# Optimization experiments

Measured on AMD Instinct MI355X. Metric: run time of the kernel, lower is better.

The kernel has to match this reference:

```python
import jax, jax.numpy as jnp
import numpy as np

D_MODEL = 1024
NUM_HEADS = 16
DIM_KEY = D_MODEL // NUM_HEADS
B, S = 2, 2048


def setup_inputs() -> dict:
    key = jax.random.key(0)
    ks = jax.random.split(key, 11)
    s = 1.0 / np.sqrt(D_MODEL)
    inp = {
        "query": jax.random.normal(ks[0], (B, S, D_MODEL), jnp.float32),
        "key": jax.random.normal(ks[1], (B, S, D_MODEL), jnp.float32),
        "value": jax.random.normal(ks[2], (B, S, D_MODEL), jnp.float32),
        "W_q": jax.random.uniform(ks[3], (D_MODEL, D_MODEL), jnp.float32, -s, s),
        "b_q": jax.random.uniform(ks[4], (D_MODEL,), jnp.float32, -s, s),
        "W_k": jax.random.uniform(ks[5], (D_MODEL, D_MODEL), jnp.float32, -s, s),
        "b_k": jax.random.uniform(ks[6], (D_MODEL,), jnp.float32, -s, s),
        "W_v": jax.random.uniform(ks[7], (D_MODEL, D_MODEL), jnp.float32, -s, s),
        "b_v": jax.random.uniform(ks[8], (D_MODEL,), jnp.float32, -s, s),
        "W_o": jax.random.uniform(ks[9], (D_MODEL, D_MODEL), jnp.float32, -s, s),
        "b_o": jax.random.uniform(ks[10], (D_MODEL,), jnp.float32, -s, s),
    }
    return inp


def _split_heads(x):
    # [B, S, D] -> [B, H, S, dk]
    b, s, _ = x.shape
    return x.reshape(b, s, NUM_HEADS, DIM_KEY).transpose(0, 2, 1, 3)


def reference(query, key, value, W_q, b_q, W_k, b_k, W_v, b_v, W_o, b_o):
    # torch Linear: y = x @ W^T + b
    q = _split_heads(query @ W_q.T + b_q)   # [B,H,S,dk]
    k = _split_heads(key @ W_k.T + b_k)
    v = _split_heads(value @ W_v.T + b_v)
    scale = 1.0 / np.sqrt(DIM_KEY).astype(np.float32)
    scores = jnp.einsum("bhqd,bhkd->bhqk", q, k) * scale  # [B,H,S,S]
    probs = jax.nn.softmax(scores, axis=-1)
    attn = jnp.einsum("bhqk,bhkd->bhqd", probs, v)        # [B,H,S,dk]
    combined = attn.transpose(0, 2, 1, 3).reshape(query.shape[0], query.shape[1], D_MODEL)
    return combined @ W_o.T + b_o
```

## Files before the change

kernel.cpp:

```cpp
#include <hip/hip_runtime.h>
#include <stdint.h>


typedef float f32x4 __attribute__((ext_vector_type(4)));
typedef __bf16 bf16x8 __attribute__((ext_vector_type(8)));
typedef unsigned short u16;

__device__ __forceinline__ u16 f2bf(float x){
  unsigned u = __float_as_uint(x);
  u += 0x7fffu + ((u>>16)&1u);
  return (u16)(u>>16);
}
__device__ __forceinline__ unsigned cvt_pk_bf16(float a, float b){
  unsigned r;
  asm("v_cvt_pk_bf16_f32 %0, %1, %2" : "=v"(r) : "v"(a), "v"(b));
  return r;
}
__device__ __forceinline__ void glds16(const void* g, void* l){
  __builtin_amdgcn_global_load_lds((__attribute__((address_space(1))) void*)g,
                                   (__attribute__((address_space(3))) void*)l, 16, 0, 0);
}
#define MFMA16(a,b,c) __builtin_amdgcn_mfma_f32_16x16x32_bf16(a,b,c,0,0,0)

__global__ __launch_bounds__(256) void cvt_all(
    const float* __restrict__ q, const float* __restrict__ k, const float* __restrict__ v,
    const float* __restrict__ wq, const float* __restrict__ wk, const float* __restrict__ wv,
    const float* __restrict__ wo, u16* __restrict__ ws)
{
  size_t g = ((size_t)blockIdx.x*256 + threadIdx.x)*4;
  int seg = (int)(g >> 20);
  const float* src; size_t base;
  if      (seg <  4){ src=q;  base=(size_t)0u;       }
  else if (seg <  8){ src=k;  base=(size_t)4u<<20;   }
  else if (seg < 12){ src=v;  base=(size_t)8u<<20;   }
  else if (seg ==12){ src=wq; base=(size_t)12u<<20;  }
  else if (seg ==13){ src=wk; base=(size_t)13u<<20;  }
  else if (seg ==14){ src=wv; base=(size_t)14u<<20;  }
  else              { src=wo; base=(size_t)15u<<20;  }
  float4 val = *(const float4*)(src + (g - base));
  uint2 o; o.x = cvt_pk_bf16(val.x, val.y); o.y = cvt_pk_bf16(val.z, val.w);
  *(uint2*)(ws + g) = o;
}

template<int MODE>
__device__ __forceinline__ void gemm_core(const u16* __restrict__ A, const u16* __restrict__ Wt,
                                          const float* __restrict__ bias, u16* outB, float* outF,
                                          float scale)
{
  __shared__ __align__(16) u16 As[128*32];
  __shared__ __align__(16) u16 Bs[128*32];
  const int tid  = threadIdx.x;
  const int lane = tid & 63, w = tid >> 6;
  const int quad = lane >> 4, l15 = lane & 15;
  const int m0 = blockIdx.y*128, n0 = blockIdx.x*128;
  const int wm = (w>>1)*64, wn = (w&1)*64;
  const int sw = (l15>>1)&3;

  f32x4 acc[4][4];
  #pragma unroll
  for (int i=0;i<4;i++)
    #pragma unroll
    for (int j=0;j<4;j++) acc[i][j] = (f32x4){0.f,0.f,0.f,0.f};

  for (int kt = 0; kt < 1024; kt += 32){
    #pragma unroll
    for (int t=0;t<2;t++){
      int id = t*256 + tid;
      int r = id>>2;
      int gc = (id&3) ^ ((id>>3)&3);
      glds16(A  + (size_t)(m0+r)*1024 + kt + gc*8, (void*)&As[id*8]);
      glds16(Wt + (size_t)(n0+r)*1024 + kt + gc*8, (void*)&Bs[id*8]);
    }
    __syncthreads();
    bf16x8 af[4], bfv[4];
    #pragma unroll
    for (int i=0;i<4;i++) af[i]  = *(const bf16x8*)&As[(wm + i*16 + l15)*32 + (quad^sw)*8];
    #pragma unroll
    for (int j=0;j<4;j++) bfv[j] = *(const bf16x8*)&Bs[(wn + j*16 + l15)*32 + (quad^sw)*8];
    #pragma unroll
    for (int i=0;i<4;i++)
      #pragma unroll
      for (int j=0;j<4;j++)
        acc[i][j] = MFMA16(af[i], bfv[j], acc[i][j]);
    __syncthreads();
  }

  #pragma unroll
  for (int i=0;i<4;i++)
    #pragma unroll
    for (int j=0;j<4;j++)
      #pragma unroll
      for (int r=0;r<4;r++){
        int row = m0 + wm + i*16 + quad*4 + r;
        int col = n0 + wn + j*16 + l15;
        float vv = (acc[i][j][r] + bias[col]) * scale;
        if (MODE==0){
          size_t o = ((size_t)((row>>11)*16 + (col>>6))*2048 + (row&2047))*64 + (col&63);
          outB[o] = f2bf(vv);
        } else {
          outF[(size_t)row*1024 + col] = vv;
        }
      }
}

__global__ __launch_bounds__(256,3) void gemm_qkv(
  const u16* __restrict__ Xq, const u16* __restrict__ Xk, const u16* __restrict__ Xv,
  const u16* __restrict__ Wq, const u16* __restrict__ Wk, const u16* __restrict__ Wv,
  const float* __restrict__ bq, const float* __restrict__ bk, const float* __restrict__ bv,
  u16* __restrict__ Qh, u16* __restrict__ Kh, u16* __restrict__ Vh)
{
  const int z = blockIdx.z;
  const u16*  A  = (z==0)?Xq:(z==1)?Xk:Xv;
  const u16*  Wt = (z==0)?Wq:(z==1)?Wk:Wv;
  const float* b = (z==0)?bq:(z==1)?bk:bv;
  u16*        O  = (z==0)?Qh:(z==1)?Kh:Vh;
  gemm_core<0>(A, Wt, b, O, nullptr, (z==0)?0.1803368801111243f:1.0f);
}

__global__ __launch_bounds__(256,3) void gemm_out(
  const u16* __restrict__ comb, const u16* __restrict__ Wo,
  const float* __restrict__ bo, float* __restrict__ out)
{
  gemm_core<1>(comb, Wo, bo, nullptr, out, 1.0f);
}

__global__ __launch_bounds__(256) void transpose_v(const u16* __restrict__ V, u16* __restrict__ Vt){
  __shared__ u16 t[64*65];
  const int bh = blockIdx.y, s0 = blockIdx.x*64;
  #pragma unroll
  for (int it=0; it<16; it++){
    int id = it*256 + threadIdx.x;
    int r = id>>6, c = id&63;
    t[c*65 + r] = V[((size_t)bh*2048 + s0 + r)*64 + c];
  }
  __syncthreads();
  #pragma unroll
  for (int it=0; it<16; it++){
    int id = it*256 + threadIdx.x;
    int d = id>>6, sc = id&63;
    Vt[((size_t)bh*64 + d)*2048 + s0 + sc] = t[d*65 + sc];
  }
}

__global__ __launch_bounds__(256,2) void attn(
  const u16* __restrict__ Q, const u16* __restrict__ K, const u16* __restrict__ Vt,
  u16* __restrict__ comb)
{
  __shared__ __align__(16) u16 K_s[128*64];
  __shared__ __align__(16) u16 V_s[64*128];
  __shared__ __align__(16) u16 P_s[128*128];
  const int tid = threadIdx.x;
  const int lane = tid&63, w = tid>>6, quad = lane>>4, l15 = lane&15;
  const int l7 = l15&7;
  const int bh = blockIdx.y, q0 = blockIdx.x*128;
  const u16* Qb = Q  + ((size_t)bh*2048 + q0)*64;
  const u16* Kb = K  + (size_t)bh*2048*64;
  const u16* Vb = Vt + (size_t)bh*64*2048;

  #pragma unroll
  for (int it=0; it<4; it++){
    int id = it*256 + tid;
    int gc = (id&7) ^ ((id>>3)&7);
    glds16(Qb + (size_t)(id>>3)*64 + gc*8, (void*)&P_s[id*8]);
  }
  __syncthreads();
  bf16x8 qa[2][2];
  #pragma unroll
  for (int c2=0; c2<2; c2++)
    #pragma unroll
    for (int ks=0; ks<2; ks++)
      qa[c2][ks] = *(const bf16x8*)&P_s[(w*32 + c2*16 + l15)*64 + ((ks*4+quad)^l7)*8];
  __syncthreads();

  const __bf16 one1 = (__bf16)1.0f;
  const bf16x8 ones = (bf16x8){one1,one1,one1,one1,one1,one1,one1,one1};

  f32x4 O[2][4];
  #pragma unroll
  for (int rt=0; rt<2; rt++)
    #pragma unroll
    for (int dt=0; dt<4; dt++) O[rt][dt] = (f32x4){0.f,0.f,0.f,0.f};
  f32x4 lacc[2] = {(f32x4){0.f,0.f,0.f,0.f}, (f32x4){0.f,0.f,0.f,0.f}};

  for (int t=0; t<16; t++){
    const int kv0 = t*128;
    #pragma unroll
    for (int it=0; it<4; it++){
      int id = it*256 + tid;
      int gck = (id&7)  ^ ((id>>3)&7);
      int gcv = (id&15) ^ ((id>>4)&15);
      glds16(Kb + (size_t)(kv0 + (id>>3))*64 + gck*8, (void*)&K_s[id*8]);
      glds16(Vb + (size_t)(id>>4)*2048 + kv0 + gcv*8, (void*)&V_s[id*8]);
    }
    __syncthreads();

    #pragma unroll
    for (int r8=0; r8<8; r8++){
      bf16x8 ka0 = *(const bf16x8*)&K_s[(r8*16 + l15)*64 + ((0+quad)^l7)*8];
      bf16x8 ka1 = *(const bf16x8*)&K_s[(r8*16 + l15)*64 + ((4+quad)^l7)*8];
      #pragma unroll
      for (int c2=0; c2<2; c2++){
        f32x4 s = (f32x4){0.f,0.f,0.f,0.f};
        s = MFMA16(ka0, qa[c2][0], s);
        s = MFMA16(ka1, qa[c2][1], s);
        int qq   = w*32 + c2*16 + l15;
        int chnk = (r8*2 + (quad>>1)) ^ l15;
        int off  = qq*128 + chnk*8 + (quad&1)*4;
        uint2 pw;
        pw.x = cvt_pk_bf16(__builtin_amdgcn_exp2f(s[0]), __builtin_amdgcn_exp2f(s[1]));
        pw.y = cvt_pk_bf16(__builtin_amdgcn_exp2f(s[2]), __builtin_amdgcn_exp2f(s[3]));
        *(uint2*)&P_s[off] = pw;
      }
    }

    bf16x8 pa[2][4];
    #pragma unroll
    for (int rt=0; rt<2; rt++)
      #pragma unroll
      for (int kk=0; kk<4; kk++){
        int qq   = w*32 + rt*16 + l15;
        int chnk = (kk*4 + quad) ^ l15;
        pa[rt][kk] = *(const bf16x8*)&P_s[qq*128 + chnk*8];
      }
    #pragma unroll
    for (int kk=0; kk<4; kk++){
      lacc[0] = MFMA16(pa[0][kk], ones, lacc[0]);
      lacc[1] = MFMA16(pa[1][kk], ones, lacc[1]);
    }
    #pragma unroll
    for (int dt=0; dt<4; dt++)
      #pragma unroll
      for (int kk=0; kk<4; kk++){
        bf16x8 vb = *(const bf16x8*)&V_s[(dt*16 + l15)*128 + (((kk*4+quad)^l15))*8];
        O[0][dt] = MFMA16(pa[0][kk], vb, O[0][dt]);
        O[1][dt] = MFMA16(pa[1][kk], vb, O[1][dt]);
      }
    __syncthreads();
  }

  const int b = bh>>4, h = bh&15;
  #pragma unroll
  for (int rt=0; rt<2; rt++)
    #pragma unroll
    for (int i=0;i<4;i++){
      float inv = 1.0f/lacc[rt][i];
      int qrow  = q0 + w*32 + rt*16 + quad*4 + i;
      #pragma unroll
      for (int dt=0; dt<4; dt++){
        size_t o = ((size_t)b*2048 + qrow)*1024 + (size_t)h*64 + dt*16 + l15;
        comb[o] = f2bf(O[rt][dt][i] * inv);
      }
    }
}

extern "C" void kernel_launch(void* const* d_in, const int* in_sizes, int n_in,
                              void* d_out, int out_size, void* d_ws, size_t ws_size,
                              hipStream_t stream)
{
  const float* q  = (const float*)d_in[0];
  const float* k  = (const float*)d_in[1];
  const float* v  = (const float*)d_in[2];
  const float* Wq = (const float*)d_in[3];
  const float* bq = (const float*)d_in[4];
  const float* Wk = (const float*)d_in[5];
  const float* bk = (const float*)d_in[6];
  const float* Wv = (const float*)d_in[7];
  const float* bv = (const float*)d_in[8];
  const float* Wo = (const float*)d_in[9];
  const float* bo = (const float*)d_in[10];
  float* out = (float*)d_out;

  u16* ws  = (u16*)d_ws;
  u16* Xq  = ws;
  u16* Xk  = ws + ((size_t)4u<<20);
  u16* Xv  = ws + ((size_t)8u<<20);
  u16* Wqb = ws + ((size_t)12u<<20);
  u16* Wkb = ws + ((size_t)13u<<20);
  u16* Wvb = ws + ((size_t)14u<<20);
  u16* Wob = ws + ((size_t)15u<<20);
  u16* Qh  = ws + ((size_t)16u<<20);
  u16* Kh  = ws + ((size_t)20u<<20);
  u16* Vh  = ws + ((size_t)24u<<20);
  u16* Vth  = Xk;
  u16* comb = Xq;

  cvt_all<<<16384, 256, 0, stream>>>(q, k, v, Wq, Wk, Wv, Wo, ws);
  gemm_qkv<<<dim3(8,32,3), 256, 0, stream>>>(Xq, Xk, Xv, Wqb, Wkb, Wvb, bq, bk, bv, Qh, Kh, Vh);
  transpose_v<<<dim3(32,32), 256, 0, stream>>>(Vh, Vth);
  attn<<<dim3(16,32), 256, 0, stream>>>(Qh, Kh, Vth, comb);
  gemm_out<<<dim3(8,32), 256, 0, stream>>>(comb, Wob, bo, out);
}
```

Measured before the change: 229.1 us.

## Fuse fp32-to-bf16 conversion into GEMM loads and write V transposed directly

Removes the separate conversion kernel by having the GEMMs load fp32 inputs and weights and convert them to bf16 before storing to shared memory. It also drops the transpose_v kernel by having the V projection write its output already transposed into the layout attention expects. This cuts two kernel launches and a full round trip of the activations through global memory. In exchange the GEMM loads become synchronous register loads instead of direct global-to-LDS transfers, and each weight is re-read in fp32 and reconverted by every tile that uses it.

After: 256.3 us. 11.9% more time.

```diff
diff --git a/kernel.cpp b/kernel.cpp
--- a/kernel.cpp
+++ b/kernel.cpp
@@ -22,30 +22,12 @@
 }
 #define MFMA16(a,b,c) __builtin_amdgcn_mfma_f32_16x16x32_bf16(a,b,c,0,0,0)
 
-__global__ __launch_bounds__(256) void cvt_all(
-    const float* __restrict__ q, const float* __restrict__ k, const float* __restrict__ v,
-    const float* __restrict__ wq, const float* __restrict__ wk, const float* __restrict__ wv,
-    const float* __restrict__ wo, u16* __restrict__ ws)
-{
-  size_t g = ((size_t)blockIdx.x*256 + threadIdx.x)*4;
-  int seg = (int)(g >> 20);
-  const float* src; size_t base;
-  if      (seg <  4){ src=q;  base=(size_t)0u;       }
-  else if (seg <  8){ src=k;  base=(size_t)4u<<20;   }
-  else if (seg < 12){ src=v;  base=(size_t)8u<<20;   }
-  else if (seg ==12){ src=wq; base=(size_t)12u<<20;  }
-  else if (seg ==13){ src=wk; base=(size_t)13u<<20;  }
-  else if (seg ==14){ src=wv; base=(size_t)14u<<20;  }
-  else              { src=wo; base=(size_t)15u<<20;  }
-  float4 val = *(const float4*)(src + (g - base));
-  uint2 o; o.x = cvt_pk_bf16(val.x, val.y); o.y = cvt_pk_bf16(val.z, val.w);
-  *(uint2*)(ws + g) = o;
-}
-
-template<int MODE>
-__device__ __forceinline__ void gemm_core(const u16* __restrict__ A, const u16* __restrict__ Wt,
-                                          const float* __restrict__ bias, u16* outB, float* outF,
-                                          float scale)
+template<bool CA, bool CB>
+__device__ __forceinline__ void gemm_core(const void* __restrict__ Aptr,
+                                          const void* __restrict__ Bptr,
+                                          const float* __restrict__ bias,
+                                          int mode, float scale,
+                                          u16* __restrict__ outB, float* __restrict__ outF)
 {
   __shared__ __align__(16) u16 As[128*32];
   __shared__ __align__(16) u16 Bs[128*32];
@@ -68,8 +50,26 @@
       int id = t*256 + tid;
       int r = id>>2;
       int gc = (id&3) ^ ((id>>3)&3);
-      glds16(A  + (size_t)(m0+r)*1024 + kt + gc*8, (void*)&As[id*8]);
-      glds16(Wt + (size_t)(n0+r)*1024 + kt + gc*8, (void*)&Bs[id*8]);
+      size_t ga = (size_t)(m0+r)*1024 + kt + gc*8;
+      size_t gb = (size_t)(n0+r)*1024 + kt + gc*8;
+      if (CA){
+        const float* g = (const float*)Aptr + ga;
+        float4 x0 = *(const float4*)g, x1 = *(const float4*)(g+4);
+        uint4 pk; pk.x = cvt_pk_bf16(x0.x,x0.y); pk.y = cvt_pk_bf16(x0.z,x0.w);
+                  pk.z = cvt_pk_bf16(x1.x,x1.y); pk.w = cvt_pk_bf16(x1.z,x1.w);
+        *(uint4*)&As[id*8] = pk;
+      } else {
+        glds16((const u16*)Aptr + ga, (void*)&As[id*8]);
+      }
+      if (CB){
+        const float* g = (const float*)Bptr + gb;
+        float4 x0 = *(const float4*)g, x1 = *(const float4*)(g+4);
+        uint4 pk; pk.x = cvt_pk_bf16(x0.x,x0.y); pk.y = cvt_pk_bf16(x0.z,x0.w);
+                  pk.z = cvt_pk_bf16(x1.x,x1.y); pk.w = cvt_pk_bf16(x1.z,x1.w);
+        *(uint4*)&Bs[id*8] = pk;
+      } else {
+        glds16((const u16*)Bptr + gb, (void*)&Bs[id*8]);
+      }
     }
     __syncthreads();
     bf16x8 af[4], bfv[4];
@@ -85,61 +85,60 @@
     __syncthreads();
   }
 
-  #pragma unroll
-  for (int i=0;i<4;i++)
-    #pragma unroll
-    for (int j=0;j<4;j++)
-      #pragma unroll
-      for (int r=0;r<4;r++){
-        int row = m0 + wm + i*16 + quad*4 + r;
+  if (mode == 2){
+    #pragma unroll
+    for (int i=0;i<4;i++)
+      #pragma unroll
+      for (int j=0;j<4;j++){
+        int row = m0 + wm + i*16 + quad*4;
         int col = n0 + wn + j*16 + l15;
-        float vv = (acc[i][j][r] + bias[col]) * scale;
-        if (MODE==0){
-          size_t o = ((size_t)((row>>11)*16 + (col>>6))*2048 + (row&2047))*64 + (col&63);
-          outB[o] = f2bf(vv);
-        } else {
-          outF[(size_t)row*1024 + col] = vv;
+        float bc = bias[col];
+        uint2 pk;
+        pk.x = cvt_pk_bf16(acc[i][j][0]+bc, acc[i][j][1]+bc);
+        pk.y = cvt_pk_bf16(acc[i][j][2]+bc, acc[i][j][3]+bc);
+        int bh = ((row>>11)<<4) + (col>>6);
+        size_t o = ((size_t)bh*64 + (col&63))*2048 + (row&2047);
+        *(uint2*)(outB + o) = pk;
+      }
+  } else {
+    #pragma unroll
+    for (int i=0;i<4;i++)
+      #pragma unroll
+      for (int j=0;j<4;j++)
+        #pragma unroll
+        for (int r=0;r<4;r++){
+          int row = m0 + wm + i*16 + quad*4 + r;
+          int col = n0 + wn + j*16 + l15;
+          float vv = (acc[i][j][r] + bias[col]) * scale;
+          if (mode==0){
+            size_t o = ((size_t)((row>>11)*16 + (col>>6))*2048 + (row&2047))*64 + (col&63);
+            outB[o] = f2bf(vv);
+          } else {
+            outF[(size_t)row*1024 + col] = vv;
+          }
         }
-      }
+  }
 }
 
 __global__ __launch_bounds__(256,3) void gemm_qkv(
-  const u16* __restrict__ Xq, const u16* __restrict__ Xk, const u16* __restrict__ Xv,
-  const u16* __restrict__ Wq, const u16* __restrict__ Wk, const u16* __restrict__ Wv,
+  const float* __restrict__ q, const float* __restrict__ k, const float* __restrict__ v,
+  const float* __restrict__ wq, const float* __restrict__ wk, const float* __restrict__ wv,
   const float* __restrict__ bq, const float* __restrict__ bk, const float* __restrict__ bv,
-  u16* __restrict__ Qh, u16* __restrict__ Kh, u16* __restrict__ Vh)
+  u16* __restrict__ Qh, u16* __restrict__ Kh, u16* __restrict__ Vt)
 {
   const int z = blockIdx.z;
-  const u16*  A  = (z==0)?Xq:(z==1)?Xk:Xv;
-  const u16*  Wt = (z==0)?Wq:(z==1)?Wk:Wv;
-  const float* b = (z==0)?bq:(z==1)?bk:bv;
-  u16*        O  = (z==0)?Qh:(z==1)?Kh:Vh;
-  gemm_core<0>(A, Wt, b, O, nullptr, (z==0)?0.1803368801111243f:1.0f);
+  const float* A  = (z==0)?q:(z==1)?k:v;
+  const float* W  = (z==0)?wq:(z==1)?wk:wv;
+  const float* bi = (z==0)?bq:(z==1)?bk:bv;
+  u16*         O  = (z==0)?Qh:(z==1)?Kh:Vt;
+  gemm_core<true,true>(A, W, bi, (z==2)?2:0, (z==0)?0.1803368801111243f:1.0f, O, nullptr);
 }
 
 __global__ __launch_bounds__(256,3) void gemm_out(
-  const u16* __restrict__ comb, const u16* __restrict__ Wo,
+  const u16* __restrict__ comb, const float* __restrict__ Wo,
   const float* __restrict__ bo, float* __restrict__ out)
 {
-  gemm_core<1>(comb, Wo, bo, nullptr, out, 1.0f);
-}
-
-__global__ __launch_bounds__(256) void transpose_v(const u16* __restrict__ V, u16* __restrict__ Vt){
-  __shared__ u16 t[64*65];
-  const int bh = blockIdx.y, s0 = blockIdx.x*64;
-  #pragma unroll
-  for (int it=0; it<16; it++){
-    int id = it*256 + threadIdx.x;
-    int r = id>>6, c = id&63;
-    t[c*65 + r] = V[((size_t)bh*2048 + s0 + r)*64 + c];
-  }
-  __syncthreads();
-  #pragma unroll
-  for (int it=0; it<16; it++){
-    int id = it*256 + threadIdx.x;
-    int d = id>>6, sc = id&63;
-    Vt[((size_t)bh*64 + d)*2048 + s0 + sc] = t[d*65 + sc];
-  }
+  gemm_core<false,true>(comb, Wo, bo, 1, 1.0f, nullptr, out);
 }
 
 __global__ __launch_bounds__(256,2) void attn(
@@ -270,23 +269,13 @@
   const float* bo = (const float*)d_in[10];
   float* out = (float*)d_out;
 
-  u16* ws  = (u16*)d_ws;
-  u16* Xq  = ws;
-  u16* Xk  = ws + ((size_t)4u<<20);
-  u16* Xv  = ws + ((size_t)8u<<20);
-  u16* Wqb = ws + ((size_t)12u<<20);
-  u16* Wkb = ws + ((size_t)13u<<20);
-  u16* Wvb = ws + ((size_t)14u<<20);
-  u16* Wob = ws + ((size_t)15u<<20);
-  u16* Qh  = ws + ((size_t)16u<<20);
-  u16* Kh  = ws + ((size_t)20u<<20);
-  u16* Vh  = ws + ((size_t)24u<<20);
-  u16* Vth  = Xk;
-  u16* comb = Xq;
-
-  cvt_all<<<16384, 256, 0, stream>>>(q, k, v, Wq, Wk, Wv, Wo, ws);
-  gemm_qkv<<<dim3(8,32,3), 256, 0, stream>>>(Xq, Xk, Xv, Wqb, Wkb, Wvb, bq, bk, bv, Qh, Kh, Vh);
-  transpose_v<<<dim3(32,32), 256, 0, stream>>>(Vh, Vth);
-  attn<<<dim3(16,32), 256, 0, stream>>>(Qh, Kh, Vth, comb);
-  gemm_out<<<dim3(8,32), 256, 0, stream>>>(comb, Wob, bo, out);
-}
+  u16* ws   = (u16*)d_ws;
+  u16* Qh   = ws;
+  u16* Kh   = ws + ((size_t)4u<<20);
+  u16* Vt   = ws + ((size_t)8u<<20);
+  u16* comb = ws + ((size_t)12u<<20);
+
+  gemm_qkv<<<dim3(8,32,3), 256, 0, stream>>>(q, k, v, Wq, Wk, Wv, bq, bk, bv, Qh, Kh, Vt);
+  attn<<<dim3(16,32), 256, 0, stream>>>(Qh, Kh, Vt, comb);
+  gemm_out<<<dim3(8,32), 256, 0, stream>>>(comb, Wo, bo, out);
+}
```

## Fuse V transpose into QKV GEMM epilogue and retile output GEMM to 64x128

Applied to the files above, without the earlier changes.

The V projection now writes its result directly in the transposed [bh, d, s] layout from the GEMM epilogue, using packed bf16x4 stores along the sequence dimension. This removes the separate transpose_v kernel and its extra global round trip. The output projection gets its own 64x128 tile kernel, which doubles the block count (512 blocks) so the 256 CUs are better filled, at the cost of more reloads of Wo. The V epilogue stores may be less coalesced, since each lane writes 8 bytes at a large stride.

Result: faster. 223.0 us (-2.7%).

```diff
diff --git a/kernel.cpp b/kernel.cpp
--- a/kernel.cpp
+++ b/kernel.cpp
@@ -43,9 +43,9 @@
 }
 
 template<int MODE>
-__device__ __forceinline__ void gemm_core(const u16* __restrict__ A, const u16* __restrict__ Wt,
-                                          const float* __restrict__ bias, u16* outB, float* outF,
-                                          float scale)
+__device__ __forceinline__ void gemm128_core(const u16* __restrict__ A, const u16* __restrict__ Wt,
+                                             const float* __restrict__ bias, u16* __restrict__ outB,
+                                             float scale)
 {
   __shared__ __align__(16) u16 As[128*32];
   __shared__ __align__(16) u16 Bs[128*32];
@@ -85,61 +85,109 @@
     __syncthreads();
   }
 
-  #pragma unroll
-  for (int i=0;i<4;i++)
-    #pragma unroll
-    for (int j=0;j<4;j++)
-      #pragma unroll
-      for (int r=0;r<4;r++){
-        int row = m0 + wm + i*16 + quad*4 + r;
+  if (MODE == 2){
+    #pragma unroll
+    for (int i=0;i<4;i++)
+      #pragma unroll
+      for (int j=0;j<4;j++){
+        int row = m0 + wm + i*16 + quad*4;
         int col = n0 + wn + j*16 + l15;
-        float vv = (acc[i][j][r] + bias[col]) * scale;
-        if (MODE==0){
+        float bc = bias[col];
+        uint2 pk;
+        pk.x = cvt_pk_bf16(acc[i][j][0]+bc, acc[i][j][1]+bc);
+        pk.y = cvt_pk_bf16(acc[i][j][2]+bc, acc[i][j][3]+bc);
+        int bh = ((row>>11)<<4) + (col>>6);
+        size_t o = ((size_t)bh*64 + (col&63))*2048 + (row&2047);
+        *(uint2*)(outB + o) = pk;
+      }
+  } else {
+    #pragma unroll
+    for (int i=0;i<4;i++)
+      #pragma unroll
+      for (int j=0;j<4;j++)
+        #pragma unroll
+        for (int r=0;r<4;r++){
+          int row = m0 + wm + i*16 + quad*4 + r;
+          int col = n0 + wn + j*16 + l15;
+          float vv = (acc[i][j][r] + bias[col]) * scale;
           size_t o = ((size_t)((row>>11)*16 + (col>>6))*2048 + (row&2047))*64 + (col&63);
           outB[o] = f2bf(vv);
-        } else {
-          outF[(size_t)row*1024 + col] = vv;
         }
-      }
+  }
 }
 
 __global__ __launch_bounds__(256,3) void gemm_qkv(
   const u16* __restrict__ Xq, const u16* __restrict__ Xk, const u16* __restrict__ Xv,
   const u16* __restrict__ Wq, const u16* __restrict__ Wk, const u16* __restrict__ Wv,
   const float* __restrict__ bq, const float* __restrict__ bk, const float* __restrict__ bv,
-  u16* __restrict__ Qh, u16* __restrict__ Kh, u16* __restrict__ Vh)
+  u16* __restrict__ Qh, u16* __restrict__ Kh, u16* __restrict__ Vt)
 {
   const int z = blockIdx.z;
-  const u16*  A  = (z==0)?Xq:(z==1)?Xk:Xv;
-  const u16*  Wt = (z==0)?Wq:(z==1)?Wk:Wv;
-  const float* b = (z==0)?bq:(z==1)?bk:bv;
-  u16*        O  = (z==0)?Qh:(z==1)?Kh:Vh;
-  gemm_core<0>(A, Wt, b, O, nullptr, (z==0)?0.1803368801111243f:1.0f);
-}
-
-__global__ __launch_bounds__(256,3) void gemm_out(
+  if (z == 2){
+    gemm128_core<2>(Xv, Wv, bv, Vt, 1.0f);
+  } else if (z == 1){
+    gemm128_core<0>(Xk, Wk, bk, Kh, 1.0f);
+  } else {
+    gemm128_core<0>(Xq, Wq, bq, Qh, 0.1803368801111243f);
+  }
+}
+
+__global__ __launch_bounds__(256,2) void gemm_out(
   const u16* __restrict__ comb, const u16* __restrict__ Wo,
   const float* __restrict__ bo, float* __restrict__ out)
 {
-  gemm_core<1>(comb, Wo, bo, nullptr, out, 1.0f);
-}
-
-__global__ __launch_bounds__(256) void transpose_v(const u16* __restrict__ V, u16* __restrict__ Vt){
-  __shared__ u16 t[64*65];
-  const int bh = blockIdx.y, s0 = blockIdx.x*64;
-  #pragma unroll
-  for (int it=0; it<16; it++){
-    int id = it*256 + threadIdx.x;
-    int r = id>>6, c = id&63;
-    t[c*65 + r] = V[((size_t)bh*2048 + s0 + r)*64 + c];
-  }
-  __syncthreads();
-  #pragma unroll
-  for (int it=0; it<16; it++){
-    int id = it*256 + threadIdx.x;
-    int d = id>>6, sc = id&63;
-    Vt[((size_t)bh*64 + d)*2048 + s0 + sc] = t[d*65 + sc];
-  }
+  __shared__ __align__(16) u16 As[64*32];
+  __shared__ __align__(16) u16 Bs[128*32];
+  const int tid  = threadIdx.x;
+  const int lane = tid & 63, w = tid >> 6;
+  const int quad = lane >> 4, l15 = lane & 15;
+  const int m0 = blockIdx.y*64, n0 = blockIdx.x*128;
+  const int sw = (l15>>1)&3;
+
+  f32x4 acc[4][2];
+  #pragma unroll
+  for (int i=0;i<4;i++)
+    #pragma unroll
+    for (int j=0;j<2;j++) acc[i][j] = (f32x4){0.f,0.f,0.f,0.f};
+
+  for (int kt = 0; kt < 1024; kt += 32){
+    {
+      int id = tid;
+      int r = id>>2;
+      int gc = (id&3) ^ ((id>>3)&3);
+      glds16(comb + (size_t)(m0+r)*1024 + kt + gc*8, (void*)&As[id*8]);
+    }
+    #pragma unroll
+    for (int t=0;t<2;t++){
+      int id = t*256 + tid;
+      int r = id>>2;
+      int gc = (id&3) ^ ((id>>3)&3);
+      glds16(Wo + (size_t)(n0+r)*1024 + kt + gc*8, (void*)&Bs[id*8]);
+    }
+    __syncthreads();
+    bf16x8 af[4], bfv[2];
+    #pragma unroll
+    for (int i=0;i<4;i++) af[i]  = *(const bf16x8*)&As[(i*16 + l15)*32 + (quad^sw)*8];
+    #pragma unroll
+    for (int j=0;j<2;j++) bfv[j] = *(const bf16x8*)&Bs[(w*32 + j*16 + l15)*32 + (quad^sw)*8];
+    #pragma unroll
+    for (int i=0;i<4;i++)
+      #pragma unroll
+      for (int j=0;j<2;j++)
+        acc[i][j] = MFMA16(af[i], bfv[j], acc[i][j]);
+    __syncthreads();
+  }
+
+  #pragma unroll
+  for (int i=0;i<4;i++)
+    #pragma unroll
+    for (int j=0;j<2;j++)
+      #pragma unroll
+      for (int r=0;r<4;r++){
+        int row = m0 + i*16 + quad*4 + r;
+        int col = n0 + w*32 + j*16 + l15;
+        out[(size_t)row*1024 + col] = acc[i][j][r] + bo[col];
+      }
 }
 
 __global__ __launch_bounds__(256,2) void attn(
@@ -280,13 +328,11 @@
   u16* Wob = ws + ((size_t)15u<<20);
   u16* Qh  = ws + ((size_t)16u<<20);
   u16* Kh  = ws + ((size_t)20u<<20);
-  u16* Vh  = ws + ((size_t)24u<<20);
-  u16* Vth  = Xk;
+  u16* Vt  = ws + ((size_t)24u<<20);
   u16* comb = Xq;
 
   cvt_all<<<16384, 256, 0, stream>>>(q, k, v, Wq, Wk, Wv, Wo, ws);
-  gemm_qkv<<<dim3(8,32,3), 256, 0, stream>>>(Xq, Xk, Xv, Wqb, Wkb, Wvb, bq, bk, bv, Qh, Kh, Vh);
-  transpose_v<<<dim3(32,32), 256, 0, stream>>>(Vh, Vth);
-  attn<<<dim3(16,32), 256, 0, stream>>>(Qh, Kh, Vth, comb);
-  gemm_out<<<dim3(8,32), 256, 0, stream>>>(comb, Wob, bo, out);
-}
+  gemm_qkv<<<dim3(8,32,3), 256, 0, stream>>>(Xq, Xk, Xv, Wqb, Wkb, Wvb, bq, bk, bv, Qh, Kh, Vt);
+  attn<<<dim3(16,32), 256, 0, stream>>>(Qh, Kh, Vt, comb);
+  gemm_out<<<dim3(8,64), 256, 0, stream>>>(comb, Wob, bo, out);
+}
```
